# Performance work log

Measured on AMD Instinct MI355X. Metric: run time of the kernel, lower is better.

The kernel has to match this reference:

```python
import jax, jax.numpy as jnp
import numpy as np

MAX_DEPTH = 20.0
VALID_THRESHOLD = 1e-6
MIN_VALID_POINTS = 10
DET_EPS = 1e-8


def setup_inputs() -> dict:
    key = jax.random.key(0)
    k1, k2 = jax.random.split(key)
    non_scale_dense = jax.random.uniform(k1, (16, 4, 768, 1024), dtype=jnp.float32)
    sparse_depth = jax.random.uniform(k2, (16, 1, 768, 1024), dtype=jnp.float32)
    return {"non_scale_dense": non_scale_dense, "sparse_depth": sparse_depth}


def _forward(nsd, sparse):
    # nsd: [B,C,H,W], sparse: [B,1,H,W] -> squeezed to [B,H,W]
    sp = sparse[:, 0]
    mask = (sp > VALID_THRESHOLD) & (sp <= MAX_DEPTH)        # [B,H,W] bool
    mf = mask.astype(nsd.dtype)
    n = mf.sum(axis=(1, 2))                                   # [B]

    m4 = mf[:, None]                                          # [B,1,H,W]
    x_sum = (nsd * m4).sum(axis=(2, 3))                       # [B,C]
    x_sq_sum = (nsd * nsd * m4).sum(axis=(2, 3))              # [B,C]
    y_sum = (sp * mf).sum(axis=(1, 2))                        # [B]
    xy_sum = (nsd * (sp[:, None] * m4)).sum(axis=(2, 3))      # [B,C]

    nB = n[:, None]                                           # [B,1]
    det = nB * x_sq_sum - x_sum * x_sum                       # [B,C]
    # batch is skipped entirely if count < min_valid_points; channel skipped if near-singular
    ok = (nB >= MIN_VALID_POINTS) & (jnp.abs(det) >= DET_EPS)
    safe_det = jnp.where(ok, det, 1.0)
    scales = jnp.where(ok, (nB * xy_sum - x_sum * y_sum[:, None]) / safe_det, 1.0)
    biases = jnp.where(ok, (x_sq_sum * y_sum[:, None] - x_sum * xy_sum) / safe_det, 0.0)

    corrected = jnp.clip(scales[:, :, None, None] * nsd + biases[:, :, None, None], 0.0, MAX_DEPTH)

    # per-channel MSE on valid pixels
    err = (corrected - sp[:, None]) ** 2 * m4                 # [B,C,H,W]
    mse = err.sum(axis=(2, 3)) / jnp.maximum(nB, 1.0)         # [B,C]
    mse = jnp.where(nB > 0, mse, jnp.inf)
    best_idx = jnp.argmin(mse, axis=1)                        # [B]
    best_corrected = jnp.take_along_axis(corrected, best_idx[:, None, None, None], axis=1)  # [B,1,H,W]
    return corrected, best_corrected, best_idx


def reference(non_scale_dense, sparse_depth):
    return _forward(non_scale_dense, sparse_depth)
```

## Files before the change

### kernel.cpp

```cpp
#include <hip/hip_runtime.h>


typedef float f4 __attribute__((ext_vector_type(4)));

#define HWPIX (768 * 1024)
#define HW4   (HWPIX / 4)
#define CHUNKS 128
#define F4PC  (HW4 / CHUNKS)
#define ITERS (F4PC / 256)
#define VALID_THR 1e-6f
#define MAXD 20.0f
#define NPART 2048

__device__ inline double wave_sum64(double v) {
#pragma unroll
    for (int o = 32; o > 0; o >>= 1) v += __shfl_down(v, o, 64);
    return v;
}

__global__ __launch_bounds__(256) void k_reduce(const f4* __restrict__ nsd,
                                                const f4* __restrict__ sp,
                                                double* __restrict__ part) {
    const int blk = blockIdx.x;
    const int b = blk >> 7;
    const int chunk = blk & (CHUNKS - 1);
    const int t = threadIdx.x;
    const int sbase = b * HW4 + chunk * F4PC;

    float lnv = 0.f, lyv = 0.f;
    float lx[4] = {0, 0, 0, 0}, lx2[4] = {0, 0, 0, 0}, lxy[4] = {0, 0, 0, 0};
#pragma unroll
    for (int i = 0; i < ITERS; i++) {
        const int o = i * 256 + t;
        f4 s4 = sp[sbase + o];
        float mv[4], svm[4];
#pragma unroll
        for (int l = 0; l < 4; l++) {
            float sv = s4[l];
            mv[l] = (sv > VALID_THR && sv <= MAXD) ? 1.0f : 0.0f;
            svm[l] = sv * mv[l];
            lnv += mv[l];
            lyv += svm[l];
        }
#pragma unroll
        for (int c = 0; c < 4; c++) {
            f4 x4 = nsd[(b * 4 + c) * HW4 + chunk * F4PC + o];
#pragma unroll
            for (int l = 0; l < 4; l++) {
                float xv = x4[l];
                lx[c]  = fmaf(xv, mv[l], lx[c]);
                lx2[c] = fmaf(xv * xv, mv[l], lx2[c]);
                lxy[c] = fmaf(xv, svm[l], lxy[c]);
            }
        }
    }

    double vals[14] = {(double)lnv, (double)lyv,
                       (double)lx[0],  (double)lx[1],  (double)lx[2],  (double)lx[3],
                       (double)lx2[0], (double)lx2[1], (double)lx2[2], (double)lx2[3],
                       (double)lxy[0], (double)lxy[1], (double)lxy[2], (double)lxy[3]};
    __shared__ double red[4][14];
    const int wv = t >> 6, lane = t & 63;
#pragma unroll
    for (int j = 0; j < 14; j++) {
        double r = wave_sum64(vals[j]);
        if (lane == 0) red[wv][j] = r;
    }
    __syncthreads();
    if (t < 14) {
        part[t * NPART + blk] = red[0][t] + red[1][t] + red[2][t] + red[3][t];
    }
}

__global__ void k_solve(const double* __restrict__ part, float* __restrict__ wsf,
                        double* __restrict__ wsn) {
    const int t = threadIdx.x;
    const int j = t >> 6, lane = t & 63;
    const int b = lane >> 2, p = lane & 3;
    __shared__ double sred[14][16];

    double s = 0.0;
#pragma unroll
    for (int k = 0; k < 32; k++)
        s += part[j * NPART + b * CHUNKS + p * 32 + k];
    s += __shfl_down(s, 2, 64);
    s += __shfl_down(s, 1, 64);
    if (p == 0) sred[j][b] = s;
    __syncthreads();

    if (t < 64) {
        const int bb = t >> 2, c = t & 3;
        double n  = sred[0][bb];
        double y  = sred[1][bb];
        double x  = sred[2 + c][bb];
        double x2 = sred[6 + c][bb];
        double xy = sred[10 + c][bb];
        double det = n * x2 - x * x;
        bool ok = (n >= 10.0) && (fabs(det) >= 1e-8);
        double sdet = ok ? det : 1.0;
        wsf[t]      = (float)(ok ? (n * xy - x * y) / sdet : 1.0);
        wsf[64 + t] = (float)(ok ? (x2 * y - x * xy) / sdet : 0.0);
        if (c == 0) wsn[bb] = n;
    }
}

__global__ __launch_bounds__(256) void k_apply(const f4* __restrict__ nsd,
                                               const f4* __restrict__ sp,
                                               const float* __restrict__ wsf,
                                               double* __restrict__ epart,
                                               f4* __restrict__ out_corr) {
    const int blk = blockIdx.x;
    const int b = blk >> 7;
    const int chunk = blk & (CHUNKS - 1);
    const int t = threadIdx.x;
    float sc[4], bi[4];
#pragma unroll
    for (int c = 0; c < 4; c++) {
        sc[c] = wsf[b * 4 + c];
        bi[c] = wsf[64 + b * 4 + c];
    }
    float lerr[4] = {0, 0, 0, 0};
    const int sbase = b * HW4 + chunk * F4PC;
#pragma unroll
    for (int i = 0; i < ITERS; i++) {
        const int o = i * 256 + t;
        f4 s4 = __builtin_nontemporal_load(&sp[sbase + o]);
        float mv[4];
#pragma unroll
        for (int l = 0; l < 4; l++)
            mv[l] = (s4[l] > VALID_THR && s4[l] <= MAXD) ? 1.0f : 0.0f;
#pragma unroll
        for (int c = 0; c < 4; c++) {
            const int off = (b * 4 + c) * HW4 + chunk * F4PC + o;
            f4 x4 = __builtin_nontemporal_load(&nsd[off]);
            f4 o4;
#pragma unroll
            for (int l = 0; l < 4; l++)
                o4[l] = fminf(fmaxf(fmaf(sc[c], x4[l], bi[c]), 0.0f), MAXD);
            __builtin_nontemporal_store(o4, &out_corr[off]);
#pragma unroll
            for (int l = 0; l < 4; l++) {
                float d = o4[l] - s4[l];
                lerr[c] = fmaf(d * d, mv[l], lerr[c]);
            }
        }
    }

    __shared__ double red[4][4];
    const int wv = t >> 6, lane = t & 63;
#pragma unroll
    for (int j = 0; j < 4; j++) {
        double r = wave_sum64((double)lerr[j]);
        if (lane == 0) red[wv][j] = r;
    }
    __syncthreads();
    if (t < 4) {
        epart[blk * 4 + t] = red[0][t] + red[1][t] + red[2][t] + red[3][t];
    }
}

__global__ void k_argmin(const double* __restrict__ epart, const double* __restrict__ wsn,
                         int* __restrict__ bidx, float* __restrict__ out_idx) {
    const int t = threadIdx.x;
    const int b = t >> 2, c = t & 3;
    __shared__ double esum[64];
    double s = 0.0;
    for (int chunk = 0; chunk < CHUNKS; chunk++)
        s += epart[(b * CHUNKS + chunk) * 4 + c];
    esum[t] = s;
    __syncthreads();
    if (t < 16) {
        double n = wsn[t];
        double nm = (n > 1.0) ? n : 1.0;
        double best = INFINITY;
        int bc = 0;
        for (int cc = 0; cc < 4; cc++) {
            double mse = (n > 0.0) ? (esum[t * 4 + cc] / nm) : INFINITY;
            if (mse < best) { best = mse; bc = cc; }
        }
        bidx[t] = bc;
        out_idx[t] = (float)bc;
    }
}

__global__ __launch_bounds__(256) void k_best(const f4* __restrict__ corr,
                                              const int* __restrict__ bidx,
                                              f4* __restrict__ out_best) {
    const int b = blockIdx.x / 192;
    const int i = blockIdx.x % 192;
    const int c = bidx[b];
    const int base = (b * 4 + c) * HW4 + i * 1024 + threadIdx.x;
    const int obase = b * HW4 + i * 1024 + threadIdx.x;
#pragma unroll
    for (int k = 0; k < 4; k++) {
        f4 v = __builtin_nontemporal_load(&corr[base + k * 256]);
        __builtin_nontemporal_store(v, &out_best[obase + k * 256]);
    }
}

extern "C" void kernel_launch(void* const* d_in, const int* in_sizes, int n_in,
                              void* d_out, int out_size, void* d_ws, size_t ws_size,
                              hipStream_t stream) {
    const f4* nsd = (const f4*)d_in[0];
    const f4* sp  = (const f4*)d_in[1];
    float* out = (float*)d_out;

    float* out_corr = out;
    float* out_best = out + 50331648;
    float* out_idx  = out + 62914560;

    double* part  = (double*)out_best;
    double* epart = (double*)out_best + 14 * NPART;

    float*  wsf  = (float*)d_ws;
    double* wsn  = (double*)((char*)d_ws + 512);
    int*    bidx = (int*)((char*)d_ws + 640);

    k_reduce<<<NPART, 256, 0, stream>>>(nsd, sp, part);
    k_solve<<<1, 896, 0, stream>>>(part, wsf, wsn);
    k_apply<<<NPART, 256, 0, stream>>>(nsd, sp, wsf, epart, (f4*)out_corr);
    k_argmin<<<1, 64, 0, stream>>>(epart, wsn, bidx, out_idx);
    k_best<<<3072, 256, 0, stream>>>((const f4*)out_corr, bidx, (f4*)out_best);
}
```

Before: 148.7 us.

## Compute per-channel MSE analytically from moments and fuse best-channel copy into apply

The reduce pass now also accumulates the sum of squared depths and the per-channel min and max of valid inputs. The solve kernel uses these to check whether the fitted affine map can clip, and if not, it gets each channel's MSE in closed form and picks the best channel before the apply pass. For batches on this fast path, apply stops reading sparse depth and writes the best channel directly, so the separate argmin kernel and the corrected→best copy go away. The non-clipping fallback keeps the old error accumulation, now via atomics. The costs are a heavier reduce kernel and possible small numerical differences in the argmin, since MSE comes from moment cancellation instead of direct summation.

```diff
diff --git a/kernel.cpp b/kernel.cpp
--- a/kernel.cpp
+++ b/kernel.cpp
@@ -11,10 +11,21 @@
 #define VALID_THR 1e-6f
 #define MAXD 20.0f
 #define NPART 2048
-
-__device__ inline double wave_sum64(double v) {
+#define NSTAT 23
+
+__device__ inline double wred_sum(double v) {
 #pragma unroll
     for (int o = 32; o > 0; o >>= 1) v += __shfl_down(v, o, 64);
+    return v;
+}
+__device__ inline double wred_min(double v) {
+#pragma unroll
+    for (int o = 32; o > 0; o >>= 1) v = fmin(v, __shfl_down(v, o, 64));
+    return v;
+}
+__device__ inline double wred_max(double v) {
+#pragma unroll
+    for (int o = 32; o > 0; o >>= 1) v = fmax(v, __shfl_down(v, o, 64));
     return v;
 }
 
@@ -27,8 +38,10 @@
     const int t = threadIdx.x;
     const int sbase = b * HW4 + chunk * F4PC;
 
-    float lnv = 0.f, lyv = 0.f;
+    float lnv = 0.f, lyv = 0.f, ly2 = 0.f;
     float lx[4] = {0, 0, 0, 0}, lx2[4] = {0, 0, 0, 0}, lxy[4] = {0, 0, 0, 0};
+    float lmn[4] = {INFINITY, INFINITY, INFINITY, INFINITY};
+    float lmx[4] = {-INFINITY, -INFINITY, -INFINITY, -INFINITY};
 #pragma unroll
     for (int i = 0; i < ITERS; i++) {
         const int o = i * 256 + t;
@@ -41,6 +54,7 @@
             svm[l] = sv * mv[l];
             lnv += mv[l];
             lyv += svm[l];
+            ly2 = fmaf(sv * sv, mv[l], ly2);
         }
 #pragma unroll
         for (int c = 0; c < 4; c++) {
@@ -51,64 +65,120 @@
                 lx[c]  = fmaf(xv, mv[l], lx[c]);
                 lx2[c] = fmaf(xv * xv, mv[l], lx2[c]);
                 lxy[c] = fmaf(xv, svm[l], lxy[c]);
+                lmn[c] = fminf(lmn[c], mv[l] != 0.f ? xv : INFINITY);
+                lmx[c] = fmaxf(lmx[c], mv[l] != 0.f ? xv : -INFINITY);
             }
         }
     }
 
-    double vals[14] = {(double)lnv, (double)lyv,
-                       (double)lx[0],  (double)lx[1],  (double)lx[2],  (double)lx[3],
-                       (double)lx2[0], (double)lx2[1], (double)lx2[2], (double)lx2[3],
-                       (double)lxy[0], (double)lxy[1], (double)lxy[2], (double)lxy[3]};
-    __shared__ double red[4][14];
+    double vals[NSTAT] = {(double)lnv, (double)lyv, (double)ly2,
+                          (double)lx[0],  (double)lx[1],  (double)lx[2],  (double)lx[3],
+                          (double)lx2[0], (double)lx2[1], (double)lx2[2], (double)lx2[3],
+                          (double)lxy[0], (double)lxy[1], (double)lxy[2], (double)lxy[3],
+                          (double)lmn[0], (double)lmn[1], (double)lmn[2], (double)lmn[3],
+                          (double)lmx[0], (double)lmx[1], (double)lmx[2], (double)lmx[3]};
+    __shared__ double red[4][NSTAT];
     const int wv = t >> 6, lane = t & 63;
 #pragma unroll
-    for (int j = 0; j < 14; j++) {
-        double r = wave_sum64(vals[j]);
+    for (int j = 0; j < NSTAT; j++) {
+        double r = (j < 15) ? wred_sum(vals[j])
+                 : (j < 19) ? wred_min(vals[j])
+                            : wred_max(vals[j]);
         if (lane == 0) red[wv][j] = r;
     }
     __syncthreads();
-    if (t < 14) {
-        part[t * NPART + blk] = red[0][t] + red[1][t] + red[2][t] + red[3][t];
+    if (t < NSTAT) {
+        double a0 = red[0][t], a1 = red[1][t], a2 = red[2][t], a3 = red[3][t];
+        double r = (t < 15) ? (a0 + a1 + a2 + a3)
+                 : (t < 19) ? fmin(fmin(a0, a1), fmin(a2, a3))
+                            : fmax(fmax(a0, a1), fmax(a2, a3));
+        part[t * NPART + blk] = r;
     }
 }
 
 __global__ void k_solve(const double* __restrict__ part, float* __restrict__ wsf,
-                        double* __restrict__ wsn) {
+                        double* __restrict__ wsn, int* __restrict__ bidx,
+                        int* __restrict__ flags, double* __restrict__ esum,
+                        float* __restrict__ out_idx) {
     const int t = threadIdx.x;
-    const int j = t >> 6, lane = t & 63;
-    const int b = lane >> 2, p = lane & 3;
-    __shared__ double sred[14][16];
-
-    double s = 0.0;
-#pragma unroll
-    for (int k = 0; k < 32; k++)
-        s += part[j * NPART + b * CHUNKS + p * 32 + k];
-    s += __shfl_down(s, 2, 64);
-    s += __shfl_down(s, 1, 64);
-    if (p == 0) sred[j][b] = s;
+    __shared__ double sred[NSTAT][16];
+    __shared__ double smse[64];
+    __shared__ int snoclip[64];
+
+    if (t < NSTAT * 16) {
+        const int j = t >> 4, b = t & 15;
+        double acc = (j < 15) ? 0.0 : (j < 19 ? INFINITY : -INFINITY);
+        for (int k = 0; k < CHUNKS; k++) {
+            double v = part[j * NPART + b * CHUNKS + k];
+            acc = (j < 15) ? (acc + v) : (j < 19 ? fmin(acc, v) : fmax(acc, v));
+        }
+        sred[j][b] = acc;
+    }
     __syncthreads();
 
     if (t < 64) {
-        const int bb = t >> 2, c = t & 3;
-        double n  = sred[0][bb];
-        double y  = sred[1][bb];
-        double x  = sred[2 + c][bb];
-        double x2 = sred[6 + c][bb];
-        double xy = sred[10 + c][bb];
+        const int b = t >> 2, c = t & 3;
+        double n   = sred[0][b];
+        double y   = sred[1][b];
+        double y2  = sred[2][b];
+        double x   = sred[3 + c][b];
+        double x2  = sred[7 + c][b];
+        double xy  = sred[11 + c][b];
+        double xmn = sred[15 + c][b];
+        double xmx = sred[19 + c][b];
         double det = n * x2 - x * x;
         bool ok = (n >= 10.0) && (fabs(det) >= 1e-8);
         double sdet = ok ? det : 1.0;
-        wsf[t]      = (float)(ok ? (n * xy - x * y) / sdet : 1.0);
-        wsf[64 + t] = (float)(ok ? (x2 * y - x * xy) / sdet : 0.0);
-        if (c == 0) wsn[bb] = n;
+        double ad = ok ? (n * xy - x * y) / sdet : 1.0;
+        double bd = ok ? (x2 * y - x * xy) / sdet : 0.0;
+        float af = (float)ad, bf = (float)bd;
+        wsf[t] = af;
+        wsf[64 + t] = bf;
+        if (c == 0) wsn[b] = n;
+        esum[t] = 0.0;
+
+        double mse;
+        int noclip;
+        if (n <= 0.0) {
+            mse = INFINITY;
+            noclip = 1;
+        } else {
+            double A = (double)af, B = (double)bf;
+            double e0 = A * xmn + B, e1 = A * xmx + B;
+            double clo = fmin(e0, e1), chi = fmax(e0, e1);
+            noclip = (clo >= 0.0 && chi <= (double)MAXD) ? 1 : 0;
+            mse = (A * A * x2 + 2.0 * A * B * x + B * B * n
+                   - 2.0 * A * xy - 2.0 * B * y + y2) / fmax(n, 1.0);
+        }
+        smse[t] = mse;
+        snoclip[t] = noclip;
+    }
+    __syncthreads();
+
+    if (t < 16) {
+        int fast = snoclip[t * 4] & snoclip[t * 4 + 1] & snoclip[t * 4 + 2] & snoclip[t * 4 + 3];
+        flags[t] = fast ? 0 : 1;
+        if (fast) {
+            double best = INFINITY;
+            int bc = 0;
+            for (int cc = 0; cc < 4; cc++) {
+                double m = smse[t * 4 + cc];
+                if (m < best) { best = m; bc = cc; }
+            }
+            bidx[t] = bc;
+            out_idx[t] = (float)bc;
+        }
     }
 }
 
 __global__ __launch_bounds__(256) void k_apply(const f4* __restrict__ nsd,
                                                const f4* __restrict__ sp,
                                                const float* __restrict__ wsf,
-                                               double* __restrict__ epart,
-                                               f4* __restrict__ out_corr) {
+                                               const int* __restrict__ bidx,
+                                               const int* __restrict__ flags,
+                                               double* __restrict__ esum,
+                                               f4* __restrict__ out_corr,
+                                               f4* __restrict__ out_best) {
     const int blk = blockIdx.x;
     const int b = blk >> 7;
     const int chunk = blk & (CHUNKS - 1);
@@ -119,8 +189,30 @@
         sc[c] = wsf[b * 4 + c];
         bi[c] = wsf[64 + b * 4 + c];
     }
+    const int sbase = b * HW4 + chunk * F4PC;
+
+    if (flags[b] == 0) {
+        const int cbest = bidx[b];
+#pragma unroll
+        for (int i = 0; i < ITERS; i++) {
+            const int o = i * 256 + t;
+#pragma unroll
+            for (int c = 0; c < 4; c++) {
+                const int off = (b * 4 + c) * HW4 + chunk * F4PC + o;
+                f4 x4 = __builtin_nontemporal_load(&nsd[off]);
+                f4 o4;
+#pragma unroll
+                for (int l = 0; l < 4; l++)
+                    o4[l] = fminf(fmaxf(fmaf(sc[c], x4[l], bi[c]), 0.0f), MAXD);
+                __builtin_nontemporal_store(o4, &out_corr[off]);
+                if (c == cbest)
+                    __builtin_nontemporal_store(o4, &out_best[sbase + o]);
+            }
+        }
+        return;
+    }
+
     float lerr[4] = {0, 0, 0, 0};
-    const int sbase = b * HW4 + chunk * F4PC;
 #pragma unroll
     for (int i = 0; i < ITERS; i++) {
         const int o = i * 256 + t;
@@ -145,51 +237,37 @@
             }
         }
     }
-
     __shared__ double red[4][4];
     const int wv = t >> 6, lane = t & 63;
 #pragma unroll
     for (int j = 0; j < 4; j++) {
-        double r = wave_sum64((double)lerr[j]);
+        double r = wred_sum((double)lerr[j]);
         if (lane == 0) red[wv][j] = r;
     }
     __syncthreads();
-    if (t < 4) {
-        epart[blk * 4 + t] = red[0][t] + red[1][t] + red[2][t] + red[3][t];
-    }
-}
-
-__global__ void k_argmin(const double* __restrict__ epart, const double* __restrict__ wsn,
-                         int* __restrict__ bidx, float* __restrict__ out_idx) {
-    const int t = threadIdx.x;
-    const int b = t >> 2, c = t & 3;
-    __shared__ double esum[64];
-    double s = 0.0;
-    for (int chunk = 0; chunk < CHUNKS; chunk++)
-        s += epart[(b * CHUNKS + chunk) * 4 + c];
-    esum[t] = s;
-    __syncthreads();
-    if (t < 16) {
-        double n = wsn[t];
-        double nm = (n > 1.0) ? n : 1.0;
-        double best = INFINITY;
-        int bc = 0;
-        for (int cc = 0; cc < 4; cc++) {
-            double mse = (n > 0.0) ? (esum[t * 4 + cc] / nm) : INFINITY;
-            if (mse < best) { best = mse; bc = cc; }
-        }
-        bidx[t] = bc;
-        out_idx[t] = (float)bc;
-    }
+    if (t < 4)
+        atomicAdd(&esum[b * 4 + t], red[0][t] + red[1][t] + red[2][t] + red[3][t]);
 }
 
 __global__ __launch_bounds__(256) void k_best(const f4* __restrict__ corr,
-                                              const int* __restrict__ bidx,
-                                              f4* __restrict__ out_best) {
+                                              const int* __restrict__ flags,
+                                              const double* __restrict__ esum,
+                                              const double* __restrict__ wsn,
+                                              f4* __restrict__ out_best,
+                                              float* __restrict__ out_idx) {
     const int b = blockIdx.x / 192;
+    if (flags[b] == 0) return;
     const int i = blockIdx.x % 192;
-    const int c = bidx[b];
-    const int base = (b * 4 + c) * HW4 + i * 1024 + threadIdx.x;
+    double n = wsn[b];
+    double nm = fmax(n, 1.0);
+    double best = INFINITY;
+    int bc = 0;
+    for (int cc = 0; cc < 4; cc++) {
+        double mse = (n > 0.0) ? (esum[b * 4 + cc] / nm) : INFINITY;
+        if (mse < best) { best = mse; bc = cc; }
+    }
+    if (i == 0 && threadIdx.x == 0) out_idx[b] = (float)bc;
+    const int base = (b * 4 + bc) * HW4 + i * 1024 + threadIdx.x;
     const int obase = b * HW4 + i * 1024 + threadIdx.x;
 #pragma unroll
     for (int k = 0; k < 4; k++) {
@@ -209,16 +287,18 @@
     float* out_best = out + 50331648;
     float* out_idx  = out + 62914560;
 
-    double* part  = (double*)out_best;
-    double* epart = (double*)out_best + 14 * NPART;
-
-    float*  wsf  = (float*)d_ws;
-    double* wsn  = (double*)((char*)d_ws + 512);
-    int*    bidx = (int*)((char*)d_ws + 640);
+    double* part = (double*)out_best;
+
+    float*  wsf   = (float*)d_ws;
+    double* wsn   = (double*)((char*)d_ws + 512);
+    int*    bidx  = (int*)((char*)d_ws + 640);
+    int*    flags = (int*)((char*)d_ws + 704);
+    double* esum  = (double*)((char*)d_ws + 768);
 
     k_reduce<<<NPART, 256, 0, stream>>>(nsd, sp, part);
-    k_solve<<<1, 896, 0, stream>>>(part, wsf, wsn);
-    k_apply<<<NPART, 256, 0, stream>>>(nsd, sp, wsf, epart, (f4*)out_corr);
-    k_argmin<<<1, 64, 0, stream>>>(epart, wsn, bidx, out_idx);
-    k_best<<<3072, 256, 0, stream>>>((const f4*)out_corr, bidx, (f4*)out_best);
-}
+    k_solve<<<1, 384, 0, stream>>>(part, wsf, wsn, bidx, flags, esum, out_idx);
+    k_apply<<<NPART, 256, 0, stream>>>(nsd, sp, wsf, bidx, flags, esum,
+                                       (f4*)out_corr, (f4*)out_best);
+    k_best<<<3072, 256, 0, stream>>>((const f4*)out_corr, flags, esum, wsn,
+                                     (f4*)out_best, out_idx);
+}
```

Result: faster. 141.8 us (-4.6%).
